# Kernel tuning notes

Measured on AMD Instinct MI355X. Metric: run time of the kernel, lower is better.

Reference implementation:

```python
import jax, jax.numpy as jnp
import numpy as np

B, N, D, H, C = 16, 196, 768, 3072, 10

def setup_inputs() -> dict:
    key = jax.random.key(0)
    ks = jax.random.split(key, 8)
    s1 = 1.0 / np.sqrt(D)
    s2 = 1.0 / np.sqrt(H)
    return {
        "x": jax.random.normal(ks[0], (B, N, D), jnp.float32),
        "y": jax.random.randint(ks[1], (B,), 0, C),
        "W1": jax.random.normal(ks[2], (H, D), jnp.float32) * s1,
        "b1": jax.random.normal(ks[3], (H,), jnp.float32) * 0.01,
        "W2": jax.random.normal(ks[4], (D, H), jnp.float32) * s2,
        "b2": jax.random.normal(ks[5], (D,), jnp.float32) * 0.01,
        "mask_fc1": jax.random.uniform(ks[6], (C, H, D), jnp.float32),
        "mask_fc2": jax.random.uniform(ks[7], (C, D, H), jnp.float32),
    }

def reference(x, y, W1, b1, W2, b2, mask_fc1, mask_fc2):
    # per-sample masked weights: [B, out, in]
    Wm1 = W1[None, :, :] * mask_fc1[y]          # [B, H, D]
    h = jnp.einsum('bni,boi->bno', x, Wm1) + b1  # [B, N, H]
    h = jax.nn.gelu(h, approximate=False)        # act (drop1/norm are identity)
    Wm2 = W2[None, :, :] * mask_fc2[y]           # [B, D, H]
    out = jnp.einsum('bni,boi->bno', h, Wm2) + b2  # [B, N, D]
    return out
```

## Files before the change

### kernel.cpp

```cpp
#include <hip/hip_runtime.h>
#include <hip/hip_bf16.h>
#include <math.h>

#define B_ 16
#define N_ 196
#define D_ 768
#define H_ 3072
#define C_ 10
#define MPAD 256

typedef __attribute__((ext_vector_type(8))) short bf16x8;
typedef __attribute__((ext_vector_type(4))) float f32x4;

__device__ __forceinline__ ushort f2bu(float f) {
    union { float f; unsigned u; } c; c.f = f;
    unsigned u = c.u;
    unsigned r = (u + 0x7FFFu + ((u >> 16) & 1u)) >> 16;
    return (ushort)r;
}

__device__ __forceinline__ void gl_lds16(const ushort* g, ushort* l) {
    __builtin_amdgcn_global_load_lds(
        (const __attribute__((address_space(1))) void*)g,
        (__attribute__((address_space(3))) void*)l, 16, 0, 0);
}

__global__ __launch_bounds__(256) void cvt_x(const float* __restrict__ x,
                                             ushort* __restrict__ xb) {
    const int i = blockIdx.x * 256 + threadIdx.x;
    const int r = i / 96;
    const int c8 = (i % 96) * 8;
    const int b = r / N_, nn = r - b * N_;
    const float4* src = reinterpret_cast<const float4*>(x + (long)r * D_ + c8);
    float4 a = src[0], bb = src[1];
    ushort t8[8] = { f2bu(a.x), f2bu(a.y), f2bu(a.z), f2bu(a.w),
                     f2bu(bb.x), f2bu(bb.y), f2bu(bb.z), f2bu(bb.w) };
    *reinterpret_cast<uint4*>(xb + ((long)b * MPAD + nn) * D_ + c8) =
        *reinterpret_cast<const uint4*>(t8);
}

template<int EPI>
__device__ __forceinline__ void gemm_core(
    const ushort* __restrict__ A0, const float* __restrict__ W,
    const float* __restrict__ M, const int* __restrict__ y,
    const float* __restrict__ bias1,
    ushort* __restrict__ hout, float* __restrict__ pout,
    int ot, int mt, int b, int sk)
{
    constexpr int K = (EPI == 0) ? D_ : H_;
    constexpr int OH = (EPI == 0) ? H_ : D_;
    constexpr int NT = 12;
    __shared__ ushort As[128][64];
    __shared__ ushort Bs[128][72];

    const int cls = y[b];
    const int tid = threadIdx.x, lane = tid & 63, wid = tid >> 6;
    const int wm = wid >> 1, wn = wid & 1;
    const int fr = lane & 15, fq = lane >> 4;
    const int lr = lane >> 3, le = (lane & 7) * 8;

    const ushort* Ab = A0 + ((long)b * MPAD + mt * 128) * K;
    const float*  Wb = W + (long)(ot * 128) * K;
    const float*  Mb = M + ((long)cls * OH + ot * 128) * K;

    const int sr0 = tid >> 2;
    const int scb = (tid & 3) * 16;

    f32x4 acc[4][4] = {};
    const int kt0 = (EPI == 0) ? 0 : sk * NT;

    #pragma unroll
    for (int t = 0; t < NT; ++t) {
        const int k0 = (kt0 + t) * 64;
        #pragma unroll
        for (int i = 0; i < 4; ++i) {
            const int r = wid * 32 + i * 8;
            gl_lds16(Ab + (long)(r + lr) * K + k0 + le, &As[r][0]);
        }
        #pragma unroll
        for (int p = 0; p < 2; ++p) {
            const int r = p * 64 + sr0;
            const float4* wp = reinterpret_cast<const float4*>(Wb + (long)r * K + k0 + scb);
            const float4* mp = reinterpret_cast<const float4*>(Mb + (long)r * K + k0 + scb);
            float4 w0 = wp[0], w1 = wp[1], w2v = wp[2], w3 = wp[3];
            float4 q0 = mp[0], q1 = mp[1], q2  = mp[2], q3 = mp[3];
            ushort ta[8] = { f2bu(w0.x*q0.x), f2bu(w0.y*q0.y), f2bu(w0.z*q0.z), f2bu(w0.w*q0.w),
                             f2bu(w1.x*q1.x), f2bu(w1.y*q1.y), f2bu(w1.z*q1.z), f2bu(w1.w*q1.w) };
            ushort tb[8] = { f2bu(w2v.x*q2.x), f2bu(w2v.y*q2.y), f2bu(w2v.z*q2.z), f2bu(w2v.w*q2.w),
                             f2bu(w3.x*q3.x), f2bu(w3.y*q3.y), f2bu(w3.z*q3.z), f2bu(w3.w*q3.w) };
            *reinterpret_cast<uint4*>(&Bs[r][scb])     = *reinterpret_cast<const uint4*>(ta);
            *reinterpret_cast<uint4*>(&Bs[r][scb + 8]) = *reinterpret_cast<const uint4*>(tb);
        }
        __syncthreads();
        #pragma unroll
        for (int kk = 0; kk < 64; kk += 32) {
            bf16x8 af[4], bf[4];
            #pragma unroll
            for (int i = 0; i < 4; ++i)
                af[i] = *reinterpret_cast<const bf16x8*>(&As[wm*64 + i*16 + fr][kk + fq*8]);
            #pragma unroll
            for (int j = 0; j < 4; ++j)
                bf[j] = *reinterpret_cast<const bf16x8*>(&Bs[wn*64 + j*16 + fr][kk + fq*8]);
            #pragma unroll
            for (int i = 0; i < 4; ++i)
                #pragma unroll
                for (int j = 0; j < 4; ++j)
                    acc[i][j] = __builtin_amdgcn_mfma_f32_16x16x32_bf16(af[i], bf[j], acc[i][j], 0, 0, 0);
        }
        __syncthreads();
    }

    if (EPI == 0) {
        #pragma unroll
        for (int j = 0; j < 4; ++j) {
            const int o = ot*128 + wn*64 + j*16 + fr;
            const float bias = bias1[o];
            #pragma unroll
            for (int i = 0; i < 4; ++i) {
                #pragma unroll
                for (int e = 0; e < 4; ++e) {
                    const int m = mt*128 + wm*64 + i*16 + fq*4 + e;
                    float v = acc[i][j][e] + bias;
                    v = 0.5f * v * (1.0f + erff(v * 0.70710678118654752f));
                    hout[((long)b * MPAD + m) * H_ + o] = f2bu(v);
                }
            }
        }
    } else {
        float* op = pout + (size_t)sk * (size_t)(B_ * N_ * D_);
        #pragma unroll
        for (int j = 0; j < 4; ++j) {
            const int o = ot*128 + wn*64 + j*16 + fr;
            #pragma unroll
            for (int i = 0; i < 4; ++i) {
                #pragma unroll
                for (int e = 0; e < 4; ++e) {
                    const int m = mt*128 + wm*64 + i*16 + fq*4 + e;
                    if (m < N_)
                        op[((long)b * N_ + m) * D_ + o] = acc[i][j][e];
                }
            }
        }
    }
}

__global__ __launch_bounds__(256) void fg1(
    const ushort* __restrict__ xb, const float* __restrict__ W1,
    const float* __restrict__ m1, const int* __restrict__ y,
    const float* __restrict__ b1, ushort* __restrict__ h)
{
    gemm_core<0>(xb, W1, m1, y, b1, h, nullptr, blockIdx.x, blockIdx.y, blockIdx.z, 0);
}

__global__ __launch_bounds__(256) void fg2(
    const ushort* __restrict__ h, const float* __restrict__ W2,
    const float* __restrict__ m2, const int* __restrict__ y,
    float* __restrict__ part)
{
    const int z = blockIdx.z;
    gemm_core<1>(h, W2, m2, y, nullptr, nullptr, part, blockIdx.x, blockIdx.y, z >> 2, z & 3);
}

__global__ __launch_bounds__(256) void reduce_k(const float* __restrict__ part,
                                                const float* __restrict__ b2,
                                                float* __restrict__ out, int SK)
{
    const int i = blockIdx.x * 256 + threadIdx.x;
    const int stride4 = B_ * N_ * D_ / 4;
    float4 s = reinterpret_cast<const float4*>(part)[i];
    for (int k = 1; k < SK; ++k) {
        float4 p = reinterpret_cast<const float4*>(part)[(size_t)k * stride4 + i];
        s.x += p.x; s.y += p.y; s.z += p.z; s.w += p.w;
    }
    const int ob = (i % (D_ / 4)) * 4;
    float4 bias = *reinterpret_cast<const float4*>(b2 + ob);
    s.x += bias.x; s.y += bias.y; s.z += bias.z; s.w += bias.w;
    reinterpret_cast<float4*>(out)[i] = s;
}

__global__ __launch_bounds__(256) void fb_gemm1(
    const float* __restrict__ x, const int* __restrict__ y,
    const float* __restrict__ W1, const float* __restrict__ b1,
    const float* __restrict__ mask1, ushort* __restrict__ h)
{
    __shared__ ushort As[128][72];
    __shared__ ushort Bs[64][72];
    const int ot = blockIdx.x, mt = blockIdx.y, b = blockIdx.z;
    const int cls = y[b];
    const int tid = threadIdx.x, lane = tid & 63, wid = tid >> 6;
    const int wm = wid >> 1, wn = wid & 1;
    const int fr = lane & 15, fq = lane >> 4;
    const int sr = tid >> 2, sc = (tid & 3) * 16;
    f32x4 acc[4][2] = {};
    const long xbase = ((long)b * N_) * D_;
    const long wbase = (long)(ot * 64) * D_;
    const long mbase = ((long)cls * H_ + ot * 64) * D_;
    for (int kt = 0; kt < D_ / 64; ++kt) {
        const int k0 = kt * 64 + sc;
        #pragma unroll
        for (int half = 0; half < 2; ++half) {
            const int r = sr + half * 64;
            const int m = mt * 128 + r;
            ushort tmp[16];
            if (m < N_) {
                const float4* src = reinterpret_cast<const float4*>(x + xbase + (long)m * D_ + k0);
                #pragma unroll
                for (int j = 0; j < 4; ++j) {
                    float4 v = src[j];
                    tmp[4*j+0]=f2bu(v.x); tmp[4*j+1]=f2bu(v.y); tmp[4*j+2]=f2bu(v.z); tmp[4*j+3]=f2bu(v.w);
                }
            } else { for (int j = 0; j < 16; ++j) tmp[j] = 0; }
            *reinterpret_cast<uint4*>(&As[r][sc])   = *reinterpret_cast<const uint4*>(&tmp[0]);
            *reinterpret_cast<uint4*>(&As[r][sc+8]) = *reinterpret_cast<const uint4*>(&tmp[8]);
        }
        {
            const float4* wsrc = reinterpret_cast<const float4*>(W1 + wbase + (long)sr * D_ + k0);
            const float4* msrc = reinterpret_cast<const float4*>(mask1 + mbase + (long)sr * D_ + k0);
            ushort tmp[16];
            #pragma unroll
            for (int j = 0; j < 4; ++j) {
                float4 wv = wsrc[j], mv = msrc[j];
                tmp[4*j+0]=f2bu(wv.x*mv.x); tmp[4*j+1]=f2bu(wv.y*mv.y);
                tmp[4*j+2]=f2bu(wv.z*mv.z); tmp[4*j+3]=f2bu(wv.w*mv.w);
            }
            *reinterpret_cast<uint4*>(&Bs[sr][sc])   = *reinterpret_cast<const uint4*>(&tmp[0]);
            *reinterpret_cast<uint4*>(&Bs[sr][sc+8]) = *reinterpret_cast<const uint4*>(&tmp[8]);
        }
        __syncthreads();
        #pragma unroll
        for (int kk = 0; kk < 64; kk += 32) {
            bf16x8 af[4], bf[2];
            #pragma unroll
            for (int i = 0; i < 4; ++i) af[i] = *reinterpret_cast<const bf16x8*>(&As[wm*64+i*16+fr][kk+fq*8]);
            #pragma unroll
            for (int j = 0; j < 2; ++j) bf[j] = *reinterpret_cast<const bf16x8*>(&Bs[wn*32+j*16+fr][kk+fq*8]);
            #pragma unroll
            for (int i = 0; i < 4; ++i)
                #pragma unroll
                for (int j = 0; j < 2; ++j)
                    acc[i][j] = __builtin_amdgcn_mfma_f32_16x16x32_bf16(af[i], bf[j], acc[i][j], 0, 0, 0);
        }
        __syncthreads();
    }
    #pragma unroll
    for (int j = 0; j < 2; ++j) {
        const int o = ot*64 + wn*32 + j*16 + fr;
        const float bias = b1[o];
        #pragma unroll
        for (int i = 0; i < 4; ++i)
            #pragma unroll
            for (int e = 0; e < 4; ++e) {
                const int m = mt*128 + wm*64 + i*16 + fq*4 + e;
                if (m < N_) {
                    float v = acc[i][j][e] + bias;
                    v = 0.5f * v * (1.0f + erff(v * 0.70710678118654752f));
                    h[(((long)b * N_) + m) * H_ + o] = f2bu(v);
                }
            }
    }
}

__global__ __launch_bounds__(256) void fb_gemm2(
    const ushort* __restrict__ h, const int* __restrict__ y,
    const float* __restrict__ W2, const float* __restrict__ b2,
    const float* __restrict__ mask2, float* __restrict__ dst,
    int split, int nkt, int add_bias)
{
    __shared__ ushort As[128][72];
    __shared__ ushort Bs[64][72];
    const int ot = blockIdx.x, mt = blockIdx.y, z = blockIdx.z;
    const int b = z / split, sk = z - b * split;
    const int cls = y[b];
    const int tid = threadIdx.x, lane = tid & 63, wid = tid >> 6;
    const int wm = wid >> 1, wn = wid & 1;
    const int fr = lane & 15, fq = lane >> 4;
    const int sr = tid >> 2, sc = (tid & 3) * 16;
    f32x4 acc[4][2] = {};
    const long hbase = ((long)b * N_) * H_;
    const long wbase = (long)(ot * 64) * H_;
    const long mbase = ((long)cls * D_ + ot * 64) * H_;
    const int kt0 = sk * nkt;
    for (int kt = kt0; kt < kt0 + nkt; ++kt) {
        const int k0 = kt * 64 + sc;
        #pragma unroll
        for (int half = 0; half < 2; ++half) {
            const int r = sr + half * 64;
            const int m = mt * 128 + r;
            if (m < N_) {
                const uint4* src = reinterpret_cast<const uint4*>(h + hbase + (long)m * H_ + k0);
                *reinterpret_cast<uint4*>(&As[r][sc])   = src[0];
                *reinterpret_cast<uint4*>(&As[r][sc+8]) = src[1];
            } else {
                uint4 z4 = {0u,0u,0u,0u};
                *reinterpret_cast<uint4*>(&As[r][sc])   = z4;
                *reinterpret_cast<uint4*>(&As[r][sc+8]) = z4;
            }
        }
        {
            const float4* wsrc = reinterpret_cast<const float4*>(W2 + wbase + (long)sr * H_ + k0);
            const float4* msrc = reinterpret_cast<const float4*>(mask2 + mbase + (long)sr * H_ + k0);
            ushort tmp[16];
            #pragma unroll
            for (int j = 0; j < 4; ++j) {
                float4 wv = wsrc[j], mv = msrc[j];
                tmp[4*j+0]=f2bu(wv.x*mv.x); tmp[4*j+1]=f2bu(wv.y*mv.y);
                tmp[4*j+2]=f2bu(wv.z*mv.z); tmp[4*j+3]=f2bu(wv.w*mv.w);
            }
            *reinterpret_cast<uint4*>(&Bs[sr][sc])   = *reinterpret_cast<const uint4*>(&tmp[0]);
            *reinterpret_cast<uint4*>(&Bs[sr][sc+8]) = *reinterpret_cast<const uint4*>(&tmp[8]);
        }
        __syncthreads();
        #pragma unroll
        for (int kk = 0; kk < 64; kk += 32) {
            bf16x8 af[4], bf[2];
            #pragma unroll
            for (int i = 0; i < 4; ++i) af[i] = *reinterpret_cast<const bf16x8*>(&As[wm*64+i*16+fr][kk+fq*8]);
            #pragma unroll
            for (int j = 0; j < 2; ++j) bf[j] = *reinterpret_cast<const bf16x8*>(&Bs[wn*32+j*16+fr][kk+fq*8]);
            #pragma unroll
            for (int i = 0; i < 4; ++i)
                #pragma unroll
                for (int j = 0; j < 2; ++j)
                    acc[i][j] = __builtin_amdgcn_mfma_f32_16x16x32_bf16(af[i], bf[j], acc[i][j], 0, 0, 0);
        }
        __syncthreads();
    }
    float* op = dst + (size_t)sk * (size_t)(B_ * N_ * D_);
    #pragma unroll
    for (int j = 0; j < 2; ++j) {
        const int o = ot*64 + wn*32 + j*16 + fr;
        const float bias = add_bias ? b2[o] : 0.0f;
        #pragma unroll
        for (int i = 0; i < 4; ++i)
            #pragma unroll
            for (int e = 0; e < 4; ++e) {
                const int m = mt*128 + wm*64 + i*16 + fq*4 + e;
                if (m < N_) op[(((long)b * N_) + m) * D_ + o] = acc[i][j][e] + bias;
            }
    }
}

extern "C" void kernel_launch(void* const* d_in, const int* in_sizes, int n_in,
                              void* d_out, int out_size, void* d_ws, size_t ws_size,
                              hipStream_t stream) {
    const float* x  = (const float*)d_in[0];
    const int*   y  = (const int*)d_in[1];
    const float* W1 = (const float*)d_in[2];
    const float* b1 = (const float*)d_in[3];
    const float* W2 = (const float*)d_in[4];
    const float* b2 = (const float*)d_in[5];
    const float* m1 = (const float*)d_in[6];
    const float* m2 = (const float*)d_in[7];
    float* out = (float*)d_out;

    const size_t xbB  = (size_t)B_ * MPAD * D_ * 2;
    const size_t hB   = (size_t)B_ * MPAD * H_ * 2;
    const size_t oB   = (size_t)B_ * N_ * D_ * 4;

    const size_t off_xb   = 0;
    const size_t off_h    = off_xb + xbB;
    const size_t off_part = off_h + hB;
    const size_t need     = off_part + 4 * oB;

    if (ws_size >= need) {
        ushort* xb  = (ushort*)((char*)d_ws + off_xb);
        ushort* h   = (ushort*)((char*)d_ws + off_h);
        float* part = (float*)((char*)d_ws + off_part);

        cvt_x<<<1176, 256, 0, stream>>>(x, xb);
        fg1<<<dim3(24, 2, 16), 256, 0, stream>>>(xb, W1, m1, y, b1, h);
        fg2<<<dim3(6, 2, 64), 256, 0, stream>>>(h, W2, m2, y, part);
        reduce_k<<<(B_ * N_ * D_ / 4) / 256, 256, 0, stream>>>(part, b2, out, 4);
    } else {
        const size_t fb_hB = (size_t)B_ * N_ * H_ * 2;
        ushort* h = (ushort*)d_ws;
        int SK = 0;
        if      (ws_size >= fb_hB + 4 * oB) SK = 4;
        else if (ws_size >= fb_hB + 2 * oB) SK = 2;
        float* part = (float*)((char*)d_ws + fb_hB);
        dim3 g1(H_ / 64, 2, B_);
        fb_gemm1<<<g1, 256, 0, stream>>>(x, y, W1, b1, m1, h);
        if (SK) {
            dim3 g2(D_ / 64, 2, B_ * SK);
            fb_gemm2<<<g2, 256, 0, stream>>>(h, y, W2, b2, m2, part, SK, 48 / SK, 0);
            reduce_k<<<(B_ * N_ * D_ / 4) / 256, 256, 0, stream>>>(part, b2, out, SK);
        } else {
            dim3 g2(D_ / 64, 2, B_);
            fb_gemm2<<<g2, 256, 0, stream>>>(h, y, W2, b2, m2, out, 1, 48, 1);
        }
    }
}
```

Baseline: 152.0 us.

## Precompute per-class masked bf16 W2 and retile fc1 to full-M tiles

A new prep kernel forms W2*mask in bf16 once per class that appears in y (skipping unused classes) and folds in the x conversion. The second GEMM then streams pre-masked bf16 weights straight into LDS with global_load_lds, instead of having each block reload fp32 W2 and mask and convert them. The first GEMM now uses 256x64 tiles so each block covers the whole padded M and reads its masked W1 slice once, rather than twice across two M tiles. The cost is an extra masked-weight write and read through workspace, plus a larger workspace requirement.

```diff
diff --git a/kernel.cpp b/kernel.cpp
--- a/kernel.cpp
+++ b/kernel.cpp
@@ -25,71 +25,85 @@
         (__attribute__((address_space(3))) void*)l, 16, 0, 0);
 }
 
-__global__ __launch_bounds__(256) void cvt_x(const float* __restrict__ x,
-                                             ushort* __restrict__ xb) {
-    const int i = blockIdx.x * 256 + threadIdx.x;
-    const int r = i / 96;
-    const int c8 = (i % 96) * 8;
-    const int b = r / N_, nn = r - b * N_;
-    const float4* src = reinterpret_cast<const float4*>(x + (long)r * D_ + c8);
-    float4 a = src[0], bb = src[1];
-    ushort t8[8] = { f2bu(a.x), f2bu(a.y), f2bu(a.z), f2bu(a.w),
-                     f2bu(bb.x), f2bu(bb.y), f2bu(bb.z), f2bu(bb.w) };
-    *reinterpret_cast<uint4*>(xb + ((long)b * MPAD + nn) * D_ + c8) =
-        *reinterpret_cast<const uint4*>(t8);
-}
-
-template<int EPI>
-__device__ __forceinline__ void gemm_core(
-    const ushort* __restrict__ A0, const float* __restrict__ W,
-    const float* __restrict__ M, const int* __restrict__ y,
-    const float* __restrict__ bias1,
-    ushort* __restrict__ hout, float* __restrict__ pout,
-    int ot, int mt, int b, int sk)
-{
-    constexpr int K = (EPI == 0) ? D_ : H_;
-    constexpr int OH = (EPI == 0) ? H_ : D_;
-    constexpr int NT = 12;
-    __shared__ ushort As[128][64];
-    __shared__ ushort Bs[128][72];
-
+__global__ __launch_bounds__(256) void prep2(
+    const float* __restrict__ x, const int* __restrict__ y,
+    const float* __restrict__ W2, const float* __restrict__ m2,
+    ushort* __restrict__ xb, ushort* __restrict__ wm2)
+{
+    const int bid = blockIdx.x;
+    const int tid = threadIdx.x;
+    if (bid < 5760) {
+        const int c = bid / 576, chunk = bid - c * 576;
+        bool used = false;
+        #pragma unroll
+        for (int t = 0; t < B_; ++t) used |= (y[t] == c);
+        if (!used) return;
+        const long n = (long)H_ * D_;
+        const long i = (long)chunk * 4096 + tid * 16;
+        const float4* wp = reinterpret_cast<const float4*>(W2 + i);
+        const float4* mp = reinterpret_cast<const float4*>(m2 + c * n + i);
+        float4 w0 = wp[0], w1 = wp[1], w2v = wp[2], w3 = wp[3];
+        float4 q0 = mp[0], q1 = mp[1], q2  = mp[2], q3 = mp[3];
+        ushort ta[8] = { f2bu(w0.x*q0.x), f2bu(w0.y*q0.y), f2bu(w0.z*q0.z), f2bu(w0.w*q0.w),
+                         f2bu(w1.x*q1.x), f2bu(w1.y*q1.y), f2bu(w1.z*q1.z), f2bu(w1.w*q1.w) };
+        ushort tb[8] = { f2bu(w2v.x*q2.x), f2bu(w2v.y*q2.y), f2bu(w2v.z*q2.z), f2bu(w2v.w*q2.w),
+                         f2bu(w3.x*q3.x), f2bu(w3.y*q3.y), f2bu(w3.z*q3.z), f2bu(w3.w*q3.w) };
+        uint4* op = reinterpret_cast<uint4*>(wm2 + c * n + i);
+        op[0] = *reinterpret_cast<const uint4*>(ta);
+        op[1] = *reinterpret_cast<const uint4*>(tb);
+    } else {
+        const int i = (bid - 5760) * 256 + tid;
+        const int r = i / 96;
+        const int c8 = (i % 96) * 8;
+        const int b = r / N_, nn = r - b * N_;
+        const float4* src = reinterpret_cast<const float4*>(x + (long)r * D_ + c8);
+        float4 a = src[0], bb = src[1];
+        ushort t8[8] = { f2bu(a.x), f2bu(a.y), f2bu(a.z), f2bu(a.w),
+                         f2bu(bb.x), f2bu(bb.y), f2bu(bb.z), f2bu(bb.w) };
+        *reinterpret_cast<uint4*>(xb + ((long)b * MPAD + nn) * D_ + c8) =
+            *reinterpret_cast<const uint4*>(t8);
+    }
+}
+
+__global__ __launch_bounds__(256) void fg1(
+    const ushort* __restrict__ xb, const float* __restrict__ W1,
+    const float* __restrict__ m1, const int* __restrict__ y,
+    const float* __restrict__ b1, ushort* __restrict__ h)
+{
+    __shared__ ushort As[256][64];
+    __shared__ ushort Bs[64][72];
+    const int ot = blockIdx.x;
+    const int b  = blockIdx.y;
     const int cls = y[b];
     const int tid = threadIdx.x, lane = tid & 63, wid = tid >> 6;
-    const int wm = wid >> 1, wn = wid & 1;
     const int fr = lane & 15, fq = lane >> 4;
     const int lr = lane >> 3, le = (lane & 7) * 8;
-
-    const ushort* Ab = A0 + ((long)b * MPAD + mt * 128) * K;
-    const float*  Wb = W + (long)(ot * 128) * K;
-    const float*  Mb = M + ((long)cls * OH + ot * 128) * K;
-
-    const int sr0 = tid >> 2;
-    const int scb = (tid & 3) * 16;
+    const int sr = tid >> 2, scb = (tid & 3) * 16;
+
+    const ushort* Ab = xb + (long)b * MPAD * D_;
+    const float*  Wb = W1 + (long)(ot * 64) * D_;
+    const float*  Mb = m1 + ((long)cls * H_ + ot * 64) * D_;
 
     f32x4 acc[4][4] = {};
-    const int kt0 = (EPI == 0) ? 0 : sk * NT;
-
-    #pragma unroll
-    for (int t = 0; t < NT; ++t) {
-        const int k0 = (kt0 + t) * 64;
-        #pragma unroll
-        for (int i = 0; i < 4; ++i) {
-            const int r = wid * 32 + i * 8;
-            gl_lds16(Ab + (long)(r + lr) * K + k0 + le, &As[r][0]);
-        }
-        #pragma unroll
-        for (int p = 0; p < 2; ++p) {
-            const int r = p * 64 + sr0;
-            const float4* wp = reinterpret_cast<const float4*>(Wb + (long)r * K + k0 + scb);
-            const float4* mp = reinterpret_cast<const float4*>(Mb + (long)r * K + k0 + scb);
+    #pragma unroll
+    for (int t = 0; t < 12; ++t) {
+        const int k0 = t * 64;
+        #pragma unroll
+        for (int i = 0; i < 8; ++i) {
+            const int r = i * 32 + wid * 8;
+            gl_lds16(Ab + (long)(r + lr) * D_ + k0 + le, &As[r][0]);
+        }
+        {
+            const float4* wp = reinterpret_cast<const float4*>(Wb + (long)sr * D_ + k0 + scb);
+            const float4* mp = reinterpret_cast<const float4*>(Mb + (long)sr * D_ + k0 + scb);
             float4 w0 = wp[0], w1 = wp[1], w2v = wp[2], w3 = wp[3];
             float4 q0 = mp[0], q1 = mp[1], q2  = mp[2], q3 = mp[3];
             ushort ta[8] = { f2bu(w0.x*q0.x), f2bu(w0.y*q0.y), f2bu(w0.z*q0.z), f2bu(w0.w*q0.w),
                              f2bu(w1.x*q1.x), f2bu(w1.y*q1.y), f2bu(w1.z*q1.z), f2bu(w1.w*q1.w) };
             ushort tb[8] = { f2bu(w2v.x*q2.x), f2bu(w2v.y*q2.y), f2bu(w2v.z*q2.z), f2bu(w2v.w*q2.w),
                              f2bu(w3.x*q3.x), f2bu(w3.y*q3.y), f2bu(w3.z*q3.z), f2bu(w3.w*q3.w) };
-            *reinterpret_cast<uint4*>(&Bs[r][scb])     = *reinterpret_cast<const uint4*>(ta);
-            *reinterpret_cast<uint4*>(&Bs[r][scb + 8]) = *reinterpret_cast<const uint4*>(tb);
+            *reinterpret_cast<uint4*>(&Bs[sr][scb])     = *reinterpret_cast<const uint4*>(ta);
+            *reinterpret_cast<uint4*>(&Bs[sr][scb + 8]) = *reinterpret_cast<const uint4*>(tb);
         }
         __syncthreads();
         #pragma unroll
@@ -97,10 +111,10 @@
             bf16x8 af[4], bf[4];
             #pragma unroll
             for (int i = 0; i < 4; ++i)
-                af[i] = *reinterpret_cast<const bf16x8*>(&As[wm*64 + i*16 + fr][kk + fq*8]);
+                af[i] = *reinterpret_cast<const bf16x8*>(&As[wid*64 + i*16 + fr][kk + fq*8]);
             #pragma unroll
             for (int j = 0; j < 4; ++j)
-                bf[j] = *reinterpret_cast<const bf16x8*>(&Bs[wn*64 + j*16 + fr][kk + fq*8]);
+                bf[j] = *reinterpret_cast<const bf16x8*>(&Bs[j*16 + fr][kk + fq*8]);
             #pragma unroll
             for (int i = 0; i < 4; ++i)
                 #pragma unroll
@@ -109,56 +123,89 @@
         }
         __syncthreads();
     }
-
-    if (EPI == 0) {
-        #pragma unroll
-        for (int j = 0; j < 4; ++j) {
-            const int o = ot*128 + wn*64 + j*16 + fr;
-            const float bias = bias1[o];
-            #pragma unroll
-            for (int i = 0; i < 4; ++i) {
+    #pragma unroll
+    for (int j = 0; j < 4; ++j) {
+        const int o = ot*64 + j*16 + fr;
+        const float bias = b1[o];
+        #pragma unroll
+        for (int i = 0; i < 4; ++i) {
+            #pragma unroll
+            for (int e = 0; e < 4; ++e) {
+                const int m = wid*64 + i*16 + fq*4 + e;
+                float v = acc[i][j][e] + bias;
+                v = 0.5f * v * (1.0f + erff(v * 0.70710678118654752f));
+                h[((long)b * MPAD + m) * H_ + o] = f2bu(v);
+            }
+        }
+    }
+}
+
+__global__ __launch_bounds__(256) void mgemm2(
+    const ushort* __restrict__ h, const ushort* __restrict__ wm2,
+    const int* __restrict__ y, float* __restrict__ part)
+{
+    __shared__ ushort As[128][64];
+    __shared__ ushort Bs[128][64];
+    const int ot = blockIdx.x;
+    const int mt = blockIdx.y;
+    const int z  = blockIdx.z;
+    const int b = z >> 2, sk = z & 3;
+    const int cls = y[b];
+    const int tid = threadIdx.x, lane = tid & 63, wid = tid >> 6;
+    const int wm = wid >> 1, wn = wid & 1;
+    const int fr = lane & 15, fq = lane >> 4;
+    const int lr = lane >> 3, le = (lane & 7) * 8;
+
+    const ushort* Ab = h + ((long)b * MPAD + mt * 128) * H_;
+    const ushort* Bb = wm2 + (long)cls * ((long)H_ * D_) + (long)(ot * 128) * H_;
+
+    f32x4 acc[4][4] = {};
+    const int kt0 = sk * 12;
+    #pragma unroll
+    for (int t = 0; t < 12; ++t) {
+        const int k0 = (kt0 + t) * 64;
+        #pragma unroll
+        for (int i = 0; i < 4; ++i) {
+            const int r = wid * 32 + i * 8;
+            gl_lds16(Ab + (long)(r + lr) * H_ + k0 + le, &As[r][0]);
+        }
+        #pragma unroll
+        for (int i = 0; i < 4; ++i) {
+            const int r = wid * 32 + i * 8;
+            gl_lds16(Bb + (long)(r + lr) * H_ + k0 + le, &Bs[r][0]);
+        }
+        __syncthreads();
+        #pragma unroll
+        for (int kk = 0; kk < 64; kk += 32) {
+            bf16x8 af[4], bf[4];
+            #pragma unroll
+            for (int i = 0; i < 4; ++i)
+                af[i] = *reinterpret_cast<const bf16x8*>(&As[wm*64 + i*16 + fr][kk + fq*8]);
+            #pragma unroll
+            for (int j = 0; j < 4; ++j)
+                bf[j] = *reinterpret_cast<const bf16x8*>(&Bs[wn*64 + j*16 + fr][kk + fq*8]);
+            #pragma unroll
+            for (int i = 0; i < 4; ++i)
                 #pragma unroll
-                for (int e = 0; e < 4; ++e) {
-                    const int m = mt*128 + wm*64 + i*16 + fq*4 + e;
-                    float v = acc[i][j][e] + bias;
-                    v = 0.5f * v * (1.0f + erff(v * 0.70710678118654752f));
-                    hout[((long)b * MPAD + m) * H_ + o] = f2bu(v);
-                }
-            }
-        }
-    } else {
-        float* op = pout + (size_t)sk * (size_t)(B_ * N_ * D_);
-        #pragma unroll
-        for (int j = 0; j < 4; ++j) {
-            const int o = ot*128 + wn*64 + j*16 + fr;
-            #pragma unroll
-            for (int i = 0; i < 4; ++i) {
-                #pragma unroll
-                for (int e = 0; e < 4; ++e) {
-                    const int m = mt*128 + wm*64 + i*16 + fq*4 + e;
-                    if (m < N_)
-                        op[((long)b * N_ + m) * D_ + o] = acc[i][j][e];
-                }
-            }
-        }
-    }
-}
-
-__global__ __launch_bounds__(256) void fg1(
-    const ushort* __restrict__ xb, const float* __restrict__ W1,
-    const float* __restrict__ m1, const int* __restrict__ y,
-    const float* __restrict__ b1, ushort* __restrict__ h)
-{
-    gemm_core<0>(xb, W1, m1, y, b1, h, nullptr, blockIdx.x, blockIdx.y, blockIdx.z, 0);
-}
-
-__global__ __launch_bounds__(256) void fg2(
-    const ushort* __restrict__ h, const float* __restrict__ W2,
-    const float* __restrict__ m2, const int* __restrict__ y,
-    float* __restrict__ part)
-{
-    const int z = blockIdx.z;
-    gemm_core<1>(h, W2, m2, y, nullptr, nullptr, part, blockIdx.x, blockIdx.y, z >> 2, z & 3);
+                for (int j = 0; j < 4; ++j)
+                    acc[i][j] = __builtin_amdgcn_mfma_f32_16x16x32_bf16(af[i], bf[j], acc[i][j], 0, 0, 0);
+        }
+        __syncthreads();
+    }
+    float* op = part + (size_t)sk * (size_t)(B_ * N_ * D_);
+    #pragma unroll
+    for (int j = 0; j < 4; ++j) {
+        const int o = ot*128 + wn*64 + j*16 + fr;
+        #pragma unroll
+        for (int i = 0; i < 4; ++i) {
+            #pragma unroll
+            for (int e = 0; e < 4; ++e) {
+                const int m = mt*128 + wm*64 + i*16 + fq*4 + e;
+                if (m < N_)
+                    op[((long)b * N_ + m) * D_ + o] = acc[i][j][e];
+            }
+        }
+    }
 }
 
 __global__ __launch_bounds__(256) void reduce_k(const float* __restrict__ part,
@@ -356,20 +403,23 @@
     const size_t xbB  = (size_t)B_ * MPAD * D_ * 2;
     const size_t hB   = (size_t)B_ * MPAD * H_ * 2;
     const size_t oB   = (size_t)B_ * N_ * D_ * 4;
+    const size_t wmB  = (size_t)C_ * H_ * D_ * 2;
 
     const size_t off_xb   = 0;
     const size_t off_h    = off_xb + xbB;
     const size_t off_part = off_h + hB;
-    const size_t need     = off_part + 4 * oB;
+    const size_t off_wm2  = off_part + 4 * oB;
+    const size_t need     = off_wm2 + wmB;
 
     if (ws_size >= need) {
         ushort* xb  = (ushort*)((char*)d_ws + off_xb);
         ushort* h   = (ushort*)((char*)d_ws + off_h);
         float* part = (float*)((char*)d_ws + off_part);
-
-        cvt_x<<<1176, 256, 0, stream>>>(x, xb);
-        fg1<<<dim3(24, 2, 16), 256, 0, stream>>>(xb, W1, m1, y, b1, h);
-        fg2<<<dim3(6, 2, 64), 256, 0, stream>>>(h, W2, m2, y, part);
+        ushort* wm2 = (ushort*)((char*)d_ws + off_wm2);
+
+        prep2<<<5760 + 1176, 256, 0, stream>>>(x, y, W2, m2, xb, wm2);
+        fg1<<<dim3(48, 16), 256, 0, stream>>>(xb, W1, m1, y, b1, h);
+        mgemm2<<<dim3(6, 2, 64), 256, 0, stream>>>(h, wm2, y, part);
         reduce_k<<<(B_ * N_ * D_ / 4) / 256, 256, 0, stream>>>(part, b2, out, 4);
     } else {
         const size_t fb_hB = (size_t)B_ * N_ * H_ * 2;
```

Measured after the change: 166.5 us. +9.5%, slower.

## Precompute masked bf16 weights per used class, then stream via LDS DMA

Applied to the files above, without the earlier changes.

Adds a prep kernel that, alongside the x conversion, multiplies W by the mask once for each class present in y and stores bf16 masked weights in workspace. The GEMM kernels then load B tiles with global_load_lds from these precomputed weights instead of each block re-reading fp32 W and mask and converting. This removes redundant fp32 mask/weight traffic and conversion work across the M tiles and batch samples sharing a class. In exchange it adds a materialization pass (up to 10 classes of 2.3M elements per layer) and extra workspace, and drops the padded LDS stride for Bs, which may cause bank conflicts.

```diff
diff --git a/kernel.cpp b/kernel.cpp
--- a/kernel.cpp
+++ b/kernel.cpp
@@ -25,34 +25,67 @@
         (__attribute__((address_space(3))) void*)l, 16, 0, 0);
 }
 
-__global__ __launch_bounds__(256) void cvt_x(const float* __restrict__ x,
-                                             ushort* __restrict__ xb) {
-    const int i = blockIdx.x * 256 + threadIdx.x;
-    const int r = i / 96;
-    const int c8 = (i % 96) * 8;
-    const int b = r / N_, nn = r - b * N_;
-    const float4* src = reinterpret_cast<const float4*>(x + (long)r * D_ + c8);
-    float4 a = src[0], bb = src[1];
-    ushort t8[8] = { f2bu(a.x), f2bu(a.y), f2bu(a.z), f2bu(a.w),
-                     f2bu(bb.x), f2bu(bb.y), f2bu(bb.z), f2bu(bb.w) };
-    *reinterpret_cast<uint4*>(xb + ((long)b * MPAD + nn) * D_ + c8) =
-        *reinterpret_cast<const uint4*>(t8);
+__global__ __launch_bounds__(256) void prep_all(
+    const float* __restrict__ x, const int* __restrict__ y,
+    const float* __restrict__ W1, const float* __restrict__ m1,
+    const float* __restrict__ W2, const float* __restrict__ m2,
+    ushort* __restrict__ xb, ushort* __restrict__ wm1, ushort* __restrict__ wm2)
+{
+    const int bid = blockIdx.x;
+    const int tid = threadIdx.x;
+    if (bid < 1176) {
+        const int i = bid * 256 + tid;
+        const int r = i / 96;
+        const int c8 = (i % 96) * 8;
+        const int b = r / N_, nn = r - b * N_;
+        const float4* src = reinterpret_cast<const float4*>(x + (long)r * D_ + c8);
+        float4 a = src[0], bb = src[1];
+        ushort t8[8] = { f2bu(a.x), f2bu(a.y), f2bu(a.z), f2bu(a.w),
+                         f2bu(bb.x), f2bu(bb.y), f2bu(bb.z), f2bu(bb.w) };
+        *reinterpret_cast<uint4*>(xb + ((long)b * MPAD + nn) * D_ + c8) =
+            *reinterpret_cast<const uint4*>(t8);
+        return;
+    }
+    const int v = bid - 1176;
+    const int layer = v / 5760;
+    const int w = v - layer * 5760;
+    const int c = w / 576, chunk = w - c * 576;
+    bool used = false;
+    #pragma unroll
+    for (int t = 0; t < B_; ++t) used |= (y[t] == c);
+    if (!used) return;
+    const float* W = layer ? W2 : W1;
+    const float* M = layer ? m2 : m1;
+    ushort*      O = layer ? wm2 : wm1;
+    const long n = (long)H_ * D_;
+    const long i = (long)chunk * 4096 + tid * 16;
+    const float4* wp = reinterpret_cast<const float4*>(W + i);
+    const float4* mp = reinterpret_cast<const float4*>(M + c * n + i);
+    float4 w0 = wp[0], w1 = wp[1], w2v = wp[2], w3 = wp[3];
+    float4 q0 = mp[0], q1 = mp[1], q2  = mp[2], q3 = mp[3];
+    ushort ta[8] = { f2bu(w0.x*q0.x), f2bu(w0.y*q0.y), f2bu(w0.z*q0.z), f2bu(w0.w*q0.w),
+                     f2bu(w1.x*q1.x), f2bu(w1.y*q1.y), f2bu(w1.z*q1.z), f2bu(w1.w*q1.w) };
+    ushort tb[8] = { f2bu(w2v.x*q2.x), f2bu(w2v.y*q2.y), f2bu(w2v.z*q2.z), f2bu(w2v.w*q2.w),
+                     f2bu(w3.x*q3.x), f2bu(w3.y*q3.y), f2bu(w3.z*q3.z), f2bu(w3.w*q3.w) };
+    uint4* op = reinterpret_cast<uint4*>(O + c * n + i);
+    op[0] = *reinterpret_cast<const uint4*>(ta);
+    op[1] = *reinterpret_cast<const uint4*>(tb);
 }
 
 template<int EPI>
-__device__ __forceinline__ void gemm_core(
-    const ushort* __restrict__ A0, const float* __restrict__ W,
-    const float* __restrict__ M, const int* __restrict__ y,
-    const float* __restrict__ bias1,
-    ushort* __restrict__ hout, float* __restrict__ pout,
-    int ot, int mt, int b, int sk)
+__global__ __launch_bounds__(256) void mgemm(
+    const ushort* __restrict__ A0, const ushort* __restrict__ Wm,
+    const int* __restrict__ y, const float* __restrict__ bias1,
+    ushort* __restrict__ hout, float* __restrict__ pout)
 {
     constexpr int K = (EPI == 0) ? D_ : H_;
-    constexpr int OH = (EPI == 0) ? H_ : D_;
-    constexpr int NT = 12;
     __shared__ ushort As[128][64];
-    __shared__ ushort Bs[128][72];
-
+    __shared__ ushort Bs[128][64];
+    const int ot = blockIdx.x;
+    const int mt = blockIdx.y;
+    const int z  = blockIdx.z;
+    const int b  = (EPI == 0) ? z : (z >> 2);
+    const int sk = (EPI == 0) ? 0 : (z & 3);
     const int cls = y[b];
     const int tid = threadIdx.x, lane = tid & 63, wid = tid >> 6;
     const int wm = wid >> 1, wn = wid & 1;
@@ -60,17 +93,12 @@
     const int lr = lane >> 3, le = (lane & 7) * 8;
 
     const ushort* Ab = A0 + ((long)b * MPAD + mt * 128) * K;
-    const float*  Wb = W + (long)(ot * 128) * K;
-    const float*  Mb = M + ((long)cls * OH + ot * 128) * K;
-
-    const int sr0 = tid >> 2;
-    const int scb = (tid & 3) * 16;
+    const ushort* Bb = Wm + (long)cls * ((long)H_ * D_) + (long)(ot * 128) * K;
 
     f32x4 acc[4][4] = {};
-    const int kt0 = (EPI == 0) ? 0 : sk * NT;
-
+    const int kt0 = sk * 12;
     #pragma unroll
-    for (int t = 0; t < NT; ++t) {
+    for (int t = 0; t < 12; ++t) {
         const int k0 = (kt0 + t) * 64;
         #pragma unroll
         for (int i = 0; i < 4; ++i) {
@@ -78,18 +106,9 @@
             gl_lds16(Ab + (long)(r + lr) * K + k0 + le, &As[r][0]);
         }
         #pragma unroll
-        for (int p = 0; p < 2; ++p) {
-            const int r = p * 64 + sr0;
-            const float4* wp = reinterpret_cast<const float4*>(Wb + (long)r * K + k0 + scb);
-            const float4* mp = reinterpret_cast<const float4*>(Mb + (long)r * K + k0 + scb);
-            float4 w0 = wp[0], w1 = wp[1], w2v = wp[2], w3 = wp[3];
-            float4 q0 = mp[0], q1 = mp[1], q2  = mp[2], q3 = mp[3];
-            ushort ta[8] = { f2bu(w0.x*q0.x), f2bu(w0.y*q0.y), f2bu(w0.z*q0.z), f2bu(w0.w*q0.w),
-                             f2bu(w1.x*q1.x), f2bu(w1.y*q1.y), f2bu(w1.z*q1.z), f2bu(w1.w*q1.w) };
-            ushort tb[8] = { f2bu(w2v.x*q2.x), f2bu(w2v.y*q2.y), f2bu(w2v.z*q2.z), f2bu(w2v.w*q2.w),
-                             f2bu(w3.x*q3.x), f2bu(w3.y*q3.y), f2bu(w3.z*q3.z), f2bu(w3.w*q3.w) };
-            *reinterpret_cast<uint4*>(&Bs[r][scb])     = *reinterpret_cast<const uint4*>(ta);
-            *reinterpret_cast<uint4*>(&Bs[r][scb + 8]) = *reinterpret_cast<const uint4*>(tb);
+        for (int i = 0; i < 4; ++i) {
+            const int r = wid * 32 + i * 8;
+            gl_lds16(Bb + (long)(r + lr) * K + k0 + le, &Bs[r][0]);
         }
         __syncthreads();
         #pragma unroll
@@ -142,23 +161,6 @@
             }
         }
     }
-}
-
-__global__ __launch_bounds__(256) void fg1(
-    const ushort* __restrict__ xb, const float* __restrict__ W1,
-    const float* __restrict__ m1, const int* __restrict__ y,
-    const float* __restrict__ b1, ushort* __restrict__ h)
-{
-    gemm_core<0>(xb, W1, m1, y, b1, h, nullptr, blockIdx.x, blockIdx.y, blockIdx.z, 0);
-}
-
-__global__ __launch_bounds__(256) void fg2(
-    const ushort* __restrict__ h, const float* __restrict__ W2,
-    const float* __restrict__ m2, const int* __restrict__ y,
-    float* __restrict__ part)
-{
-    const int z = blockIdx.z;
-    gemm_core<1>(h, W2, m2, y, nullptr, nullptr, part, blockIdx.x, blockIdx.y, z >> 2, z & 3);
 }
 
 __global__ __launch_bounds__(256) void reduce_k(const float* __restrict__ part,
@@ -356,20 +358,25 @@
     const size_t xbB  = (size_t)B_ * MPAD * D_ * 2;
     const size_t hB   = (size_t)B_ * MPAD * H_ * 2;
     const size_t oB   = (size_t)B_ * N_ * D_ * 4;
+    const size_t wmB  = (size_t)C_ * H_ * D_ * 2;
 
     const size_t off_xb   = 0;
     const size_t off_h    = off_xb + xbB;
     const size_t off_part = off_h + hB;
-    const size_t need     = off_part + 4 * oB;
+    const size_t off_wm1  = off_part + 4 * oB;
+    const size_t off_wm2  = off_wm1 + wmB;
+    const size_t need     = off_wm2 + wmB;
 
     if (ws_size >= need) {
         ushort* xb  = (ushort*)((char*)d_ws + off_xb);
         ushort* h   = (ushort*)((char*)d_ws + off_h);
         float* part = (float*)((char*)d_ws + off_part);
-
-        cvt_x<<<1176, 256, 0, stream>>>(x, xb);
-        fg1<<<dim3(24, 2, 16), 256, 0, stream>>>(xb, W1, m1, y, b1, h);
-        fg2<<<dim3(6, 2, 64), 256, 0, stream>>>(h, W2, m2, y, part);
+        ushort* wm1 = (ushort*)((char*)d_ws + off_wm1);
+        ushort* wm2 = (ushort*)((char*)d_ws + off_wm2);
+
+        prep_all<<<12696, 256, 0, stream>>>(x, y, W1, m1, W2, m2, xb, wm1, wm2);
+        mgemm<0><<<dim3(24, 2, 16), 256, 0, stream>>>(xb, wm1, y, b1, h, nullptr);
+        mgemm<1><<<dim3(6, 2, 64), 256, 0, stream>>>(h, wm2, y, nullptr, nullptr, part);
         reduce_k<<<(B_ * N_ * D_ / 4) / 256, 256, 0, stream>>>(part, b2, out, 4);
     } else {
         const size_t fb_hB = (size_t)B_ * N_ * H_ * 2;
```

Result: faster. 142.2 us, median of 2 (-6.4%).

## Group samples by class so each masked weight tile is built once per class

Applied to the files above, without the earlier changes.

Each block now owns one class and one output slice. It gathers all batch rows whose label matches that class into a row map and builds the masked bf16 weight tile for its full K range once, kept resident in LDS. It then streams 128-row chunks of activations through double-buffered LDS against that tile. This removes the repeated per-sample and per-M-tile reloading and multiplying of W*mask, which dominated global traffic. In exchange it uses a large LDS footprint (~120KB), and blocks for classes absent from the batch do nothing, so the work per block is uneven.

```diff
diff --git a/kernel.cpp b/kernel.cpp
--- a/kernel.cpp
+++ b/kernel.cpp
@@ -40,125 +40,129 @@
 }
 
 template<int EPI>
-__device__ __forceinline__ void gemm_core(
+__global__ __launch_bounds__(512) void fgc(
     const ushort* __restrict__ A0, const float* __restrict__ W,
     const float* __restrict__ M, const int* __restrict__ y,
-    const float* __restrict__ bias1,
-    ushort* __restrict__ hout, float* __restrict__ pout,
-    int ot, int mt, int b, int sk)
+    const float* __restrict__ b1, ushort* __restrict__ hout,
+    float* __restrict__ pout)
 {
-    constexpr int K = (EPI == 0) ? D_ : H_;
-    constexpr int OH = (EPI == 0) ? H_ : D_;
-    constexpr int NT = 12;
-    __shared__ ushort As[128][64];
-    __shared__ ushort Bs[128][72];
-
-    const int cls = y[b];
+    constexpr int KA = (EPI == 0) ? D_ : H_;
+    const int ot  = blockIdx.x;
+    const int cls = blockIdx.y;
+    const int sk  = (EPI == 0) ? 0 : blockIdx.z;
+
+    __shared__ ushort Bs[64][776];
+    __shared__ ushort As[2][128][64];
+    __shared__ short  rmap[3136];
+    __shared__ int    sBL[16];
+    __shared__ int    sNB;
+
     const int tid = threadIdx.x, lane = tid & 63, wid = tid >> 6;
-    const int wm = wid >> 1, wn = wid & 1;
+    const int wm = wid >> 2, wn = wid & 3;
     const int fr = lane & 15, fq = lane >> 4;
     const int lr = lane >> 3, le = (lane & 7) * 8;
 
-    const ushort* Ab = A0 + ((long)b * MPAD + mt * 128) * K;
-    const float*  Wb = W + (long)(ot * 128) * K;
-    const float*  Mb = M + ((long)cls * OH + ot * 128) * K;
-
-    const int sr0 = tid >> 2;
-    const int scb = (tid & 3) * 16;
-
-    f32x4 acc[4][4] = {};
-    const int kt0 = (EPI == 0) ? 0 : sk * NT;
+    if (tid == 0) {
+        int c = 0;
+        #pragma unroll
+        for (int b = 0; b < B_; ++b) if (y[b] == cls) sBL[c++] = b;
+        sNB = c;
+    }
+    __syncthreads();
+    const int nb = sNB;
+    if (nb == 0) return;
+    const int rows = nb * N_;
+    for (int r = tid; r < rows; r += 512) {
+        const int bb = r / N_;
+        rmap[r] = (short)(sBL[bb] * MPAD + (r - bb * N_));
+    }
 
     #pragma unroll
-    for (int t = 0; t < NT; ++t) {
-        const int k0 = (kt0 + t) * 64;
+    for (int it = 0; it < 6; ++it) {
+        const int e = it * 8192 + tid * 16;
+        const int row = e / 768;
+        const int col = e - row * 768;
+        const float4 *wp, *mp;
+        if (EPI == 0) {
+            wp = reinterpret_cast<const float4*>(W + (long)(ot * 64) * D_ + e);
+            mp = reinterpret_cast<const float4*>(M + (long)cls * ((long)H_ * D_)
+                                                   + (long)(ot * 64) * D_ + e);
+        } else {
+            wp = reinterpret_cast<const float4*>(W + (long)(ot * 64 + row) * H_ + sk * 768 + col);
+            mp = reinterpret_cast<const float4*>(M + ((long)cls * D_ + ot * 64 + row) * H_
+                                                   + sk * 768 + col);
+        }
+        float4 w0 = wp[0], w1 = wp[1], w2v = wp[2], w3 = wp[3];
+        float4 q0 = mp[0], q1 = mp[1], q2  = mp[2], q3 = mp[3];
+        ushort ta[8] = { f2bu(w0.x*q0.x), f2bu(w0.y*q0.y), f2bu(w0.z*q0.z), f2bu(w0.w*q0.w),
+                         f2bu(w1.x*q1.x), f2bu(w1.y*q1.y), f2bu(w1.z*q1.z), f2bu(w1.w*q1.w) };
+        ushort tb[8] = { f2bu(w2v.x*q2.x), f2bu(w2v.y*q2.y), f2bu(w2v.z*q2.z), f2bu(w2v.w*q2.w),
+                         f2bu(w3.x*q3.x), f2bu(w3.y*q3.y), f2bu(w3.z*q3.z), f2bu(w3.w*q3.w) };
+        ushort* d = &Bs[row][col];
+        *reinterpret_cast<uint4*>(d)     = *reinterpret_cast<const uint4*>(ta);
+        *reinterpret_cast<uint4*>(d + 8) = *reinterpret_cast<const uint4*>(tb);
+    }
+    __syncthreads();
+
+    const int nchunk = (rows + 127) >> 7;
+    const int o = ot * 64 + wn * 16 + fr;
+    const float bias = (EPI == 0) ? b1[o] : 0.0f;
+    const long colA0 = ((EPI == 0) ? 0 : sk * 768) + le;
+
+    for (int ch = 0; ch < nchunk; ++ch) {
+        const int r0 = ch * 128 + wid * 16;
+        const int ra = min(r0 + lr,     rows - 1);
+        const int rb = min(r0 + 8 + lr, rows - 1);
+        const long baseA = (long)rmap[ra] * KA + colA0;
+        const long baseB = (long)rmap[rb] * KA + colA0;
+
+        gl_lds16(A0 + baseA, &As[0][wid * 16][0]);
+        gl_lds16(A0 + baseB, &As[0][wid * 16 + 8][0]);
+        __syncthreads();
+
+        f32x4 acc[4] = {};
+        #pragma unroll
+        for (int t = 0; t < 12; ++t) {
+            const int bf = t & 1;
+            if (t < 11) {
+                gl_lds16(A0 + baseA + (t + 1) * 64, &As[bf ^ 1][wid * 16][0]);
+                gl_lds16(A0 + baseB + (t + 1) * 64, &As[bf ^ 1][wid * 16 + 8][0]);
+            }
+            #pragma unroll
+            for (int kk = 0; kk < 64; kk += 32) {
+                bf16x8 af[4], bfr;
+                #pragma unroll
+                for (int i = 0; i < 4; ++i)
+                    af[i] = *reinterpret_cast<const bf16x8*>(
+                        &As[bf][wm * 64 + i * 16 + fr][kk + fq * 8]);
+                bfr = *reinterpret_cast<const bf16x8*>(
+                        &Bs[wn * 16 + fr][t * 64 + kk + fq * 8]);
+                #pragma unroll
+                for (int i = 0; i < 4; ++i)
+                    acc[i] = __builtin_amdgcn_mfma_f32_16x16x32_bf16(af[i], bfr, acc[i], 0, 0, 0);
+            }
+            __syncthreads();
+        }
+
         #pragma unroll
         for (int i = 0; i < 4; ++i) {
-            const int r = wid * 32 + i * 8;
-            gl_lds16(Ab + (long)(r + lr) * K + k0 + le, &As[r][0]);
-        }
-        #pragma unroll
-        for (int p = 0; p < 2; ++p) {
-            const int r = p * 64 + sr0;
-            const float4* wp = reinterpret_cast<const float4*>(Wb + (long)r * K + k0 + scb);
-            const float4* mp = reinterpret_cast<const float4*>(Mb + (long)r * K + k0 + scb);
-            float4 w0 = wp[0], w1 = wp[1], w2v = wp[2], w3 = wp[3];
-            float4 q0 = mp[0], q1 = mp[1], q2  = mp[2], q3 = mp[3];
-            ushort ta[8] = { f2bu(w0.x*q0.x), f2bu(w0.y*q0.y), f2bu(w0.z*q0.z), f2bu(w0.w*q0.w),
-                             f2bu(w1.x*q1.x), f2bu(w1.y*q1.y), f2bu(w1.z*q1.z), f2bu(w1.w*q1.w) };
-            ushort tb[8] = { f2bu(w2v.x*q2.x), f2bu(w2v.y*q2.y), f2bu(w2v.z*q2.z), f2bu(w2v.w*q2.w),
-                             f2bu(w3.x*q3.x), f2bu(w3.y*q3.y), f2bu(w3.z*q3.z), f2bu(w3.w*q3.w) };
-            *reinterpret_cast<uint4*>(&Bs[r][scb])     = *reinterpret_cast<const uint4*>(ta);
-            *reinterpret_cast<uint4*>(&Bs[r][scb + 8]) = *reinterpret_cast<const uint4*>(tb);
-        }
-        __syncthreads();
-        #pragma unroll
-        for (int kk = 0; kk < 64; kk += 32) {
-            bf16x8 af[4], bf[4];
-            #pragma unroll
-            for (int i = 0; i < 4; ++i)
-                af[i] = *reinterpret_cast<const bf16x8*>(&As[wm*64 + i*16 + fr][kk + fq*8]);
-            #pragma unroll
-            for (int j = 0; j < 4; ++j)
-                bf[j] = *reinterpret_cast<const bf16x8*>(&Bs[wn*64 + j*16 + fr][kk + fq*8]);
-            #pragma unroll
-            for (int i = 0; i < 4; ++i)
-                #pragma unroll
-                for (int j = 0; j < 4; ++j)
-                    acc[i][j] = __builtin_amdgcn_mfma_f32_16x16x32_bf16(af[i], bf[j], acc[i][j], 0, 0, 0);
-        }
-        __syncthreads();
-    }
-
-    if (EPI == 0) {
-        #pragma unroll
-        for (int j = 0; j < 4; ++j) {
-            const int o = ot*128 + wn*64 + j*16 + fr;
-            const float bias = bias1[o];
-            #pragma unroll
-            for (int i = 0; i < 4; ++i) {
-                #pragma unroll
-                for (int e = 0; e < 4; ++e) {
-                    const int m = mt*128 + wm*64 + i*16 + fq*4 + e;
-                    float v = acc[i][j][e] + bias;
-                    v = 0.5f * v * (1.0f + erff(v * 0.70710678118654752f));
-                    hout[((long)b * MPAD + m) * H_ + o] = f2bu(v);
+            #pragma unroll
+            for (int e = 0; e < 4; ++e) {
+                const int gr = ch * 128 + wm * 64 + i * 16 + fq * 4 + e;
+                if (gr < rows) {
+                    const int v = rmap[gr];
+                    if (EPI == 0) {
+                        float val = acc[i][e] + bias;
+                        val = 0.5f * val * (1.0f + erff(val * 0.70710678118654752f));
+                        hout[(long)v * H_ + o] = f2bu(val);
+                    } else {
+                        float* op = pout + (size_t)sk * (size_t)(B_ * N_ * D_);
+                        op[((long)(v >> 8) * N_ + (v & 255)) * D_ + o] = acc[i][e];
+                    }
                 }
             }
         }
-    } else {
-        float* op = pout + (size_t)sk * (size_t)(B_ * N_ * D_);
-        #pragma unroll
-        for (int j = 0; j < 4; ++j) {
-            const int o = ot*128 + wn*64 + j*16 + fr;
-            #pragma unroll
-            for (int i = 0; i < 4; ++i) {
-                #pragma unroll
-                for (int e = 0; e < 4; ++e) {
-                    const int m = mt*128 + wm*64 + i*16 + fq*4 + e;
-                    if (m < N_)
-                        op[((long)b * N_ + m) * D_ + o] = acc[i][j][e];
-                }
-            }
-        }
-    }
-}
-
-__global__ __launch_bounds__(256) void fg1(
-    const ushort* __restrict__ xb, const float* __restrict__ W1,
-    const float* __restrict__ m1, const int* __restrict__ y,
-    const float* __restrict__ b1, ushort* __restrict__ h)
-{
-    gemm_core<0>(xb, W1, m1, y, b1, h, nullptr, blockIdx.x, blockIdx.y, blockIdx.z, 0);
-}
-
-__global__ __launch_bounds__(256) void fg2(
-    const ushort* __restrict__ h, const float* __restrict__ W2,
-    const float* __restrict__ m2, const int* __restrict__ y,
-    float* __restrict__ part)
-{
-    const int z = blockIdx.z;
-    gemm_core<1>(h, W2, m2, y, nullptr, nullptr, part, blockIdx.x, blockIdx.y, z >> 2, z & 3);
+    }
 }
 
 __global__ __launch_bounds__(256) void reduce_k(const float* __restrict__ part,
@@ -368,8 +372,8 @@
         float* part = (float*)((char*)d_ws + off_part);
 
         cvt_x<<<1176, 256, 0, stream>>>(x, xb);
-        fg1<<<dim3(24, 2, 16), 256, 0, stream>>>(xb, W1, m1, y, b1, h);
-        fg2<<<dim3(6, 2, 64), 256, 0, stream>>>(h, W2, m2, y, part);
+        fgc<0><<<dim3(48, C_),    512, 0, stream>>>(xb, W1, m1, y, b1, h, nullptr);
+        fgc<1><<<dim3(12, C_, 4), 512, 0, stream>>>(h,  W2, m2, y, nullptr, nullptr, part);
         reduce_k<<<(B_ * N_ * D_ / 4) / 256, 256, 0, stream>>>(part, b2, out, 4);
     } else {
         const size_t fb_hB = (size_t)B_ * N_ * H_ * 2;
```

After: 245.2 us. +61.3%, slower.
